# Kernel optimization log

Measured on AMD Instinct MI355X. Metric: run time of the kernel, lower is better.

## Reference

```python
import jax, jax.numpy as jnp
import numpy as np

NEG = -1000000000.0  # mask value used by the original module

def setup_inputs() -> dict:
    key = jax.random.key(0)
    kq, kk, kv, kl = jax.random.split(key, 4)
    B, Lq, Lk, D, Dv = 16, 2048, 2048, 64, 64
    q = jax.random.normal(kq, (B, Lq, D), dtype=jnp.float32)
    k = jax.random.normal(kk, (B, Lk, D), dtype=jnp.float32)
    v = jax.random.normal(kv, (B, Lk, Dv), dtype=jnp.float32)
    valid_len = jax.random.randint(kl, (B, Lq), 0, Lk, dtype=jnp.int32)
    return {"q": q, "k": k, "v": v, "valid_len": valid_len}

def reference(q, k, v, valid_len):
    # scores: [B, Lq, Lk]  (NOTE: original module does NOT scale by sqrt(d))
    scores = jnp.einsum('bqd,bkd->bqk', q, k)
    Lk = k.shape[1]
    # per-(batch,query) valid length masking over the key dimension
    mask = jnp.arange(Lk, dtype=valid_len.dtype)[None, None, :] < valid_len[:, :, None]
    scores = jnp.where(mask, scores, NEG)
    attn = jax.nn.softmax(scores, axis=-1)
    # dropout p=0.0 -> identity
    return jnp.einsum('bqk,bkv->bqv', attn, v)
```

## Files before the change

kernel.cpp:

```cpp
#include <hip/hip_runtime.h>

typedef _Float16 f16;
typedef __attribute__((ext_vector_type(8))) _Float16 f16x8;
typedef __attribute__((ext_vector_type(4))) _Float16 f16x4;
typedef __attribute__((ext_vector_type(4))) float f32x4;

#define NB 16
#define LSEQ 2048
#define DIM 64
#define KVB 64
#define QT 128
#define NQT (LSEQ / QT)
#define NT (LSEQ / KVB)
#define LOG2E 1.44269504088896340736f

__device__ inline f16x4 pkcvt(const f32x4 x) {
    auto a = __builtin_amdgcn_cvt_pkrtz(x[0], x[1]);
    auto b = __builtin_amdgcn_cvt_pkrtz(x[2], x[3]);
    f16x4 t; t[0]=(f16)a[0]; t[1]=(f16)a[1]; t[2]=(f16)b[0]; t[3]=(f16)b[1];
    return t;
}

__device__ inline void gload16(const void* g, void* l) {
    __builtin_amdgcn_global_load_lds(
        (const __attribute__((address_space(1))) unsigned int*)g,
        (__attribute__((address_space(3))) unsigned int*)l, 16, 0, 0);
}

__device__ __host__ inline int kappa(int p) {
    int kt = p >> 4, hi = (p >> 2) & 3, g = p & 3;
    return ((kt & 1) << 5) + (hi << 3) + ((kt >> 1) << 2) + g;
}

__global__ __launch_bounds__(256) void prep(
    const float* __restrict__ kg, const float* __restrict__ vg,
    const int* __restrict__ vlg,
    f16* __restrict__ k16, f16* __restrict__ v16, int* __restrict__ perm)
{
    const int tid = threadIdx.x;
    if (blockIdx.x < NB * NT) {
        const int b = blockIdx.x & 15, t = blockIdx.x >> 4;
        const int bt = b * NT + t;
        const float* kb_ = kg + ((size_t)b * LSEQ + t * KVB) * DIM;
        const float* vb_ = vg + ((size_t)b * LSEQ + t * KVB) * DIM;
        f16* kd = k16 + (size_t)bt * (KVB * DIM);
        f16* vd = v16 + (size_t)bt * (KVB * DIM);
#pragma unroll
        for (int it = 0; it < 4; ++it) {
            int cc = tid + it * 256;
            int row = cc >> 4, c4 = (cc & 15) * 4;
            f32x4 x = *(const f32x4*)(kb_ + kappa(row) * DIM + c4);
            *(f16x4*)(kd + row * 64 + (c4 ^ ((row & 7) * 8))) = pkcvt(x);
        }
        int kb4 = tid & 15, dvb = tid >> 4;
        f32x4 rr[4];
#pragma unroll
        for (int i = 0; i < 4; ++i)
            rr[i] = *(const f32x4*)(vb_ + (size_t)(kb4 * 4 + i) * DIM + dvb * 4);
#pragma unroll
        for (int j = 0; j < 4; ++j) {
            int dv = dvb * 4 + j;
            f32x4 col = {rr[0][j], rr[1][j], rr[2][j], rr[3][j]};
            *(f16x4*)(vd + dv * 64 + ((kb4 * 4) ^ ((dv & 7) * 8))) = pkcvt(col);
        }
    } else {
        const int b = blockIdx.x - NB * NT;
        __shared__ int hist[NT + 1];
        __shared__ int base[NT + 1];
        if (tid <= NT) hist[tid] = 0;
        __syncthreads();
        for (int q = tid; q < LSEQ; q += 256) {
            int vl = vlg[b * LSEQ + q];
            int t = (vl == 0) ? NT : ((vl + KVB - 1) >> 6);
            atomicAdd(&hist[t], 1);
        }
        __syncthreads();
        if (tid == 0) {
            int acc = 0;
            for (int t = NT; t >= 0; --t) { base[t] = acc; acc += hist[t]; }
        }
        __syncthreads();
        for (int q = tid; q < LSEQ; q += 256) {
            int vl = vlg[b * LSEQ + q];
            int t = (vl == 0) ? NT : ((vl + KVB - 1) >> 6);
            int pos = atomicAdd(&base[t], 1);
            perm[b * LSEQ + pos] = q;
        }
    }
}

__global__ __launch_bounds__(256, 4) void attn_fwd(
    const float* __restrict__ qg, const int* __restrict__ vlg,
    const f16* __restrict__ k16, const f16* __restrict__ v16,
    float* __restrict__ outg, const int* __restrict__ perm,
    f16* __restrict__ opart, float* __restrict__ mlg, int S)
{
    __shared__ alignas(16) f16 kbuf[2][KVB * 64];
    __shared__ alignas(16) f16 vbuf[2][DIM * 64];
    __shared__ int wmax[4];

    const int tid  = threadIdx.x;
    const int wid  = tid >> 6;
    const int lane = tid & 63;
    const int r    = lane & 15;
    const int hi   = lane >> 4;

    const int bid = blockIdx.x;
    const int nbs = NB * S;
    const int qt  = bid / nbs;
    const int rem = bid - qt * nbs;
    const int s   = rem >> 4;
    const int b   = rem & 15;
    const int qw  = qt * QT + wid * 16;

    const int qidxA = perm[b * LSEQ + qw + r];
    const int qidxB = perm[b * LSEQ + qw + 64 + r];
    const int vlA   = vlg[b * LSEQ + qidxA];
    const int vlB   = vlg[b * LSEQ + qidxB];

    int tq = max((vlA == 0) ? NT : ((vlA + KVB - 1) >> 6),
                 (vlB == 0) ? NT : ((vlB + KVB - 1) >> 6));
    tq = max(tq, __shfl_xor(tq, 1));
    tq = max(tq, __shfl_xor(tq, 2));
    tq = max(tq, __shfl_xor(tq, 4));
    tq = max(tq, __shfl_xor(tq, 8));
    if (lane == 0) wmax[wid] = tq;
    __syncthreads();
    const int maxt = max(max(wmax[0], wmax[1]), max(wmax[2], wmax[3]));

    auto rmin = [&](int v) {
        v = min(v, __shfl_xor(v, 1));
        v = min(v, __shfl_xor(v, 2));
        v = min(v, __shfl_xor(v, 4));
        v = min(v, __shfl_xor(v, 8));
        return v;
    };
    const int vminA = rmin(vlA);
    const int vminB = rmin(vlB);

    auto load_q = [&](int qidx, f16x8* qf) {
        const float* qrow = qg + ((size_t)(b * LSEQ + qidx)) * DIM;
#pragma unroll
        for (int ks = 0; ks < 2; ++ks) {
            f32x4 x = *(const f32x4*)(qrow + ks * 32 + hi * 8);
            f32x4 y = *(const f32x4*)(qrow + ks * 32 + hi * 8 + 4);
            f32x4 xs = {x[0]*LOG2E, x[1]*LOG2E, x[2]*LOG2E, x[3]*LOG2E};
            f32x4 ys = {y[0]*LOG2E, y[1]*LOG2E, y[2]*LOG2E, y[3]*LOG2E};
            f16x4 lo = pkcvt(xs), hh = pkcvt(ys);
            f16x8 t;
            t[0]=lo[0]; t[1]=lo[1]; t[2]=lo[2]; t[3]=lo[3];
            t[4]=hh[0]; t[5]=hh[1]; t[6]=hh[2]; t[7]=hh[3];
            qf[ks] = t;
        }
    };
    f16x8 qfA[2], qfB[2];
    load_q(qidxA, qfA);
    load_q(qidxB, qfB);

    float mA = -INFINITY, mB = -INFINITY;
    float lA = 0.0f, lB = 0.0f;
    f32x4 oA[4], oB[4];
#pragma unroll
    for (int dt = 0; dt < 4; ++dt) { oA[dt] = f32x4{0,0,0,0}; oB[dt] = f32x4{0,0,0,0}; }

    const f16* kt_base = k16 + (size_t)b * (NT * KVB * DIM);
    const f16* vt_base = v16 + (size_t)b * (NT * KVB * DIM);
    const int swz = (r & 7) * 8;

    auto stage = [&](int bi, int t) {
        const char* ks = (const char*)(kt_base + (size_t)t * 4096);
        const char* vs = (const char*)(vt_base + (size_t)t * 4096);
        char* kd = (char*)&kbuf[bi][0];
        char* vd = (char*)&vbuf[bi][0];
        gload16(ks + tid * 16,        kd + tid * 16);
        gload16(ks + 4096 + tid * 16, kd + 4096 + tid * 16);
        gload16(vs + tid * 16,        vd + tid * 16);
        gload16(vs + 4096 + tid * 16, vd + 4096 + tid * 16);
    };

    auto do_sm = [&](f32x4* st, int vl, int vmin, float& m_run, float& l_run,
                     f32x4* o, int kv0, f16x8* pa) {
        float lanemax = -INFINITY;
        if (kv0 + KVB > vmin) {
#pragma unroll
            for (int kt = 0; kt < 4; ++kt)
#pragma unroll
                for (int g = 0; g < 4; ++g) {
                    int key = kv0 + ((kt & 1) << 5) + (hi << 3) + ((kt >> 1) << 2) + g;
                    float sv = (key < vl) ? st[kt][g] : -1e9f;
                    st[kt][g] = sv;
                    lanemax = fmaxf(lanemax, sv);
                }
        } else {
#pragma unroll
            for (int kt = 0; kt < 4; ++kt)
#pragma unroll
                for (int g = 0; g < 4; ++g)
                    lanemax = fmaxf(lanemax, st[kt][g]);
        }

        if (__any(lanemax > m_run + 8.0f)) {
            float tmax = lanemax;
            tmax = fmaxf(tmax, __shfl_xor(tmax, 16));
            tmax = fmaxf(tmax, __shfl_xor(tmax, 32));
            float m_new = fmaxf(m_run, tmax);
            float scale = exp2f(m_run - m_new);
            l_run *= scale;
            m_run = m_new;
#pragma unroll
            for (int g = 0; g < 4; ++g) {
                float sc = __shfl(scale, hi * 4 + g);
#pragma unroll
                for (int dt = 0; dt < 4; ++dt) o[dt][g] *= sc;
            }
        }

#pragma unroll
        for (int kt = 0; kt < 4; ++kt)
#pragma unroll
            for (int g = 0; g < 4; ++g) {
                float p = exp2f(st[kt][g] - m_run);
                l_run += p;
                pa[kt & 1][((kt >> 1) << 2) + g] = (f16)p;
            }
    };

    if (s < maxt) stage(0, s);
    int c = 0;
    for (int tt = s; tt < maxt; tt += S) {
        __syncthreads();
        if (tt + S < maxt) stage(c ^ 1, tt + S);
        const int kv0 = tt * KVB;

        f32x4 stA[4], stB[4];
        __builtin_amdgcn_s_setprio(1);
#pragma unroll
        for (int kt = 0; kt < 4; ++kt) {
            f16x8 kf0 = *(const f16x8*)(&kbuf[c][(kt * 16 + r) * 64 + ((0 * 32 + hi * 8) ^ swz)]);
            f16x8 kf1 = *(const f16x8*)(&kbuf[c][(kt * 16 + r) * 64 + ((1 * 32 + hi * 8) ^ swz)]);
            f32x4 a = __builtin_amdgcn_mfma_f32_16x16x32_f16(kf0, qfA[0], f32x4{0,0,0,0}, 0, 0, 0);
            stA[kt] = __builtin_amdgcn_mfma_f32_16x16x32_f16(kf1, qfA[1], a, 0, 0, 0);
            f32x4 bb = __builtin_amdgcn_mfma_f32_16x16x32_f16(kf0, qfB[0], f32x4{0,0,0,0}, 0, 0, 0);
            stB[kt] = __builtin_amdgcn_mfma_f32_16x16x32_f16(kf1, qfB[1], bb, 0, 0, 0);
        }
        __builtin_amdgcn_s_setprio(0);

        f16x8 paA[2], paB[2];
        do_sm(stA, vlA, vminA, mA, lA, oA, kv0, paA);
        do_sm(stB, vlB, vminB, mB, lB, oB, kv0, paB);

        __builtin_amdgcn_s_setprio(1);
#pragma unroll
        for (int dt = 0; dt < 4; ++dt)
#pragma unroll
            for (int ks = 0; ks < 2; ++ks) {
                f16x8 vf = *(const f16x8*)(&vbuf[c][(dt * 16 + r) * 64 + ((ks * 32 + hi * 8) ^ swz)]);
                oA[dt] = __builtin_amdgcn_mfma_f32_16x16x32_f16(paA[ks], vf, oA[dt], 0, 0, 0);
                oB[dt] = __builtin_amdgcn_mfma_f32_16x16x32_f16(paB[ks], vf, oB[dt], 0, 0, 0);
            }
        __builtin_amdgcn_s_setprio(0);
        c ^= 1;
    }

    auto epi = [&](float m_run, float l_run, f32x4* o, int qidx) {
        l_run += __shfl_xor(l_run, 16);
        l_run += __shfl_xor(l_run, 32);
        if (S == 1) {
            float inv = 1.0f / l_run;
#pragma unroll
            for (int g = 0; g < 4; ++g) {
                float iv = __shfl(inv, hi * 4 + g);
                int   qo = __shfl(qidx, hi * 4 + g);
                float* ob = outg + ((size_t)(b * LSEQ + qo)) * DIM;
#pragma unroll
                for (int dt = 0; dt < 4; ++dt)
                    ob[dt * 16 + r] = o[dt][g] * iv;
            }
        } else {
            f16* obase = opart + ((size_t)s * NB * LSEQ + (size_t)b * LSEQ) * DIM;
#pragma unroll
            for (int g = 0; g < 4; ++g) {
                int qo = __shfl(qidx, hi * 4 + g);
                f16* ob = obase + (size_t)qo * DIM;
#pragma unroll
                for (int dt = 0; dt < 4; ++dt)
                    ob[dt * 16 + r] = (f16)o[dt][g];
            }
            if (hi == 0) {
                size_t mi = ((size_t)s * NB * LSEQ + (size_t)b * LSEQ + qidx) * 2;
                mlg[mi]     = m_run;
                mlg[mi + 1] = l_run;
            }
        }
    };
    epi(mA, lA, oA, qidxA);
    epi(mB, lB, oB, qidxB);
}

__global__ void merge_k(const f16* __restrict__ opart, const float* __restrict__ mlg,
                        float* __restrict__ outg, int S)
{
    const int gt = blockIdx.x * 256 + threadIdx.x;
    const size_t base = (size_t)gt * 4;
    const size_t qg = base >> 6;
    float M = -INFINITY;
    for (int s = 0; s < S; ++s)
        M = fmaxf(M, mlg[((size_t)s * NB * LSEQ + qg) * 2]);
    float den = 0.f;
    f32x4 acc = {0.f, 0.f, 0.f, 0.f};
    for (int s = 0; s < S; ++s) {
        size_t mi = ((size_t)s * NB * LSEQ + qg) * 2;
        float w = exp2f(mlg[mi] - M);
        den += w * mlg[mi + 1];
        f16x4 ov = *(const f16x4*)(opart + (size_t)s * (NB * LSEQ * DIM) + base);
        acc[0] += w * (float)ov[0]; acc[1] += w * (float)ov[1];
        acc[2] += w * (float)ov[2]; acc[3] += w * (float)ov[3];
    }
    float inv = 1.0f / den;
    f32x4 res = {acc[0]*inv, acc[1]*inv, acc[2]*inv, acc[3]*inv};
    *(f32x4*)(outg + base) = res;
}

extern "C" void kernel_launch(void* const* d_in, const int* in_sizes, int n_in,
                              void* d_out, int out_size, void* d_ws, size_t ws_size,
                              hipStream_t stream) {
    const float* q  = (const float*)d_in[0];
    const float* k  = (const float*)d_in[1];
    const float* v  = (const float*)d_in[2];
    const int*   vl = (const int*)d_in[3];
    float* out = (float*)d_out;

    const size_t perm_b = (size_t)NB * LSEQ * sizeof(int);
    const size_t kv_b   = (size_t)NB * LSEQ * DIM * sizeof(f16);
    auto need = [&](int S) {
        return perm_b + 2 * kv_b
             + (size_t)S * NB * LSEQ * 2 * sizeof(float)
             + (size_t)S * NB * LSEQ * DIM * sizeof(f16);
    };
    int S;
    if      (ws_size >= need(4)) S = 4;
    else if (ws_size >= need(2)) S = 2;
    else                         S = 1;

    int*   perm  = (int*)d_ws;
    f16*   k16   = (f16*)((char*)d_ws + perm_b);
    f16*   v16   = (f16*)((char*)d_ws + perm_b + kv_b);
    float* mlg   = (float*)((char*)d_ws + perm_b + 2 * kv_b);
    f16*   opart = (f16*)((char*)d_ws + perm_b + 2 * kv_b
                          + (size_t)S * NB * LSEQ * 2 * sizeof(float));

    prep<<<NB * NT + NB, 256, 0, stream>>>(k, v, vl, k16, v16, perm);

    attn_fwd<<<dim3(NQT * NB * S), dim3(256), 0, stream>>>(
        q, vl, k16, v16, out, perm, opart, mlg, S);

    if (S > 1) {
        const int mthreads = NB * LSEQ * DIM / 4;
        merge_k<<<dim3(mthreads / 256), dim3(256), 0, stream>>>(opart, mlg, out, S);
    }
}
```

Baseline: 46.03 us.

## Use per-query-tile variable split counts for balanced split-KV attention

Replaces the uniform split factor S with a per-query-tile table: tiles holding long valid lengths (sorted first) get up to 8 KV splits and short tiles fewer, giving 1072 blocks with more even work. Partial outputs and stats are now stored by sorted rank, so writes are contiguous, and the merge kernel scatters to the original query index through perm. The merge skips S==1 rows. This drops the workspace-size check and assumes room for 8 splits, and the merge still launches over all rows.

```diff
diff --git a/kernel.cpp b/kernel.cpp
--- a/kernel.cpp
+++ b/kernel.cpp
@@ -12,7 +12,13 @@
 #define QT 128
 #define NQT (LSEQ / QT)
 #define NT (LSEQ / KVB)
+#define SMAX 8
 #define LOG2E 1.44269504088896340736f
+
+__device__ __constant__ int STAB[NQT]     = {8,8,7,6,6,5,5,4,4,3,3,2,2,2,1,1};
+__device__ __constant__ int BTAB[NQT + 1] = {0,128,256,368,464,560,640,720,784,848,896,944,976,1008,1040,1056,1072};
+#define GRID_ATTN 1072
+static const int H_STAB[NQT] = {8,8,7,6,6,5,5,4,4,3,3,2,2,2,1,1};
 
 __device__ inline f16x4 pkcvt(const f32x4 x) {
     auto a = __builtin_amdgcn_cvt_pkrtz(x[0], x[1]);
@@ -93,7 +99,7 @@
     const float* __restrict__ qg, const int* __restrict__ vlg,
     const f16* __restrict__ k16, const f16* __restrict__ v16,
     float* __restrict__ outg, const int* __restrict__ perm,
-    f16* __restrict__ opart, float* __restrict__ mlg, int S)
+    f16* __restrict__ opart, float* __restrict__ mlg)
 {
     __shared__ alignas(16) f16 kbuf[2][KVB * 64];
     __shared__ alignas(16) f16 vbuf[2][DIM * 64];
@@ -106,15 +112,18 @@
     const int hi   = lane >> 4;
 
     const int bid = blockIdx.x;
-    const int nbs = NB * S;
-    const int qt  = bid / nbs;
-    const int rem = bid - qt * nbs;
+    int qt = 0;
+    while (bid >= BTAB[qt + 1]) ++qt;
+    const int rem = bid - BTAB[qt];
+    const int b   = rem & 15;
     const int s   = rem >> 4;
-    const int b   = rem & 15;
+    const int S   = STAB[qt];
     const int qw  = qt * QT + wid * 16;
 
-    const int qidxA = perm[b * LSEQ + qw + r];
-    const int qidxB = perm[b * LSEQ + qw + 64 + r];
+    const int rankA = qw + r;
+    const int rankB = qw + 64 + r;
+    const int qidxA = perm[b * LSEQ + rankA];
+    const int qidxB = perm[b * LSEQ + rankB];
     const int vlA   = vlg[b * LSEQ + qidxA];
     const int vlB   = vlg[b * LSEQ + qidxB];
 
@@ -262,7 +271,7 @@
         c ^= 1;
     }
 
-    auto epi = [&](float m_run, float l_run, f32x4* o, int qidx) {
+    auto epi = [&](float m_run, float l_run, f32x4* o, int qidx, int rank) {
         l_run += __shfl_xor(l_run, 16);
         l_run += __shfl_xor(l_run, 32);
         if (S == 1) {
@@ -280,36 +289,39 @@
             f16* obase = opart + ((size_t)s * NB * LSEQ + (size_t)b * LSEQ) * DIM;
 #pragma unroll
             for (int g = 0; g < 4; ++g) {
-                int qo = __shfl(qidx, hi * 4 + g);
-                f16* ob = obase + (size_t)qo * DIM;
+                int rk = __shfl(rank, hi * 4 + g);
+                f16* ob = obase + (size_t)rk * DIM;
 #pragma unroll
                 for (int dt = 0; dt < 4; ++dt)
                     ob[dt * 16 + r] = (f16)o[dt][g];
             }
             if (hi == 0) {
-                size_t mi = ((size_t)s * NB * LSEQ + (size_t)b * LSEQ + qidx) * 2;
+                size_t mi = ((size_t)s * NB * LSEQ + (size_t)b * LSEQ + rank) * 2;
                 mlg[mi]     = m_run;
                 mlg[mi + 1] = l_run;
             }
         }
     };
-    epi(mA, lA, oA, qidxA);
-    epi(mB, lB, oB, qidxB);
+    epi(mA, lA, oA, qidxA, rankA);
+    epi(mB, lB, oB, qidxB, rankB);
 }
 
 __global__ void merge_k(const f16* __restrict__ opart, const float* __restrict__ mlg,
-                        float* __restrict__ outg, int S)
+                        const int* __restrict__ perm, float* __restrict__ outg)
 {
     const int gt = blockIdx.x * 256 + threadIdx.x;
     const size_t base = (size_t)gt * 4;
-    const size_t qg = base >> 6;
+    const size_t rlin = base >> 6;
+    const int rank = (int)(rlin & (LSEQ - 1));
+    const int S = STAB[rank >> 7];
+    if (S == 1) return;
     float M = -INFINITY;
     for (int s = 0; s < S; ++s)
-        M = fmaxf(M, mlg[((size_t)s * NB * LSEQ + qg) * 2]);
+        M = fmaxf(M, mlg[((size_t)s * NB * LSEQ + rlin) * 2]);
     float den = 0.f;
     f32x4 acc = {0.f, 0.f, 0.f, 0.f};
     for (int s = 0; s < S; ++s) {
-        size_t mi = ((size_t)s * NB * LSEQ + qg) * 2;
+        size_t mi = ((size_t)s * NB * LSEQ + rlin) * 2;
         float w = exp2f(mlg[mi] - M);
         den += w * mlg[mi + 1];
         f16x4 ov = *(const f16x4*)(opart + (size_t)s * (NB * LSEQ * DIM) + base);
@@ -317,8 +329,11 @@
         acc[2] += w * (float)ov[2]; acc[3] += w * (float)ov[3];
     }
     float inv = 1.0f / den;
+    const size_t bq = (rlin >> 11);
+    const int qidx = perm[rlin];
+    float* ob = outg + ((size_t)(bq * LSEQ + qidx)) * DIM + (base & 63);
     f32x4 res = {acc[0]*inv, acc[1]*inv, acc[2]*inv, acc[3]*inv};
-    *(f32x4*)(outg + base) = res;
+    *(f32x4*)ob = res;
 }
 
 extern "C" void kernel_launch(void* const* d_in, const int* in_sizes, int n_in,
@@ -332,30 +347,22 @@
 
     const size_t perm_b = (size_t)NB * LSEQ * sizeof(int);
     const size_t kv_b   = (size_t)NB * LSEQ * DIM * sizeof(f16);
-    auto need = [&](int S) {
-        return perm_b + 2 * kv_b
-             + (size_t)S * NB * LSEQ * 2 * sizeof(float)
-             + (size_t)S * NB * LSEQ * DIM * sizeof(f16);
-    };
-    int S;
-    if      (ws_size >= need(4)) S = 4;
-    else if (ws_size >= need(2)) S = 2;
-    else                         S = 1;
+    const size_t mlg_b  = (size_t)SMAX * NB * LSEQ * 2 * sizeof(float);
+    const size_t need   = perm_b + 2 * kv_b + mlg_b
+                        + (size_t)SMAX * NB * LSEQ * DIM * sizeof(f16);
+    (void)need;
 
     int*   perm  = (int*)d_ws;
     f16*   k16   = (f16*)((char*)d_ws + perm_b);
     f16*   v16   = (f16*)((char*)d_ws + perm_b + kv_b);
     float* mlg   = (float*)((char*)d_ws + perm_b + 2 * kv_b);
-    f16*   opart = (f16*)((char*)d_ws + perm_b + 2 * kv_b
-                          + (size_t)S * NB * LSEQ * 2 * sizeof(float));
+    f16*   opart = (f16*)((char*)d_ws + perm_b + 2 * kv_b + mlg_b);
 
     prep<<<NB * NT + NB, 256, 0, stream>>>(k, v, vl, k16, v16, perm);
 
-    attn_fwd<<<dim3(NQT * NB * S), dim3(256), 0, stream>>>(
-        q, vl, k16, v16, out, perm, opart, mlg, S);
-
-    if (S > 1) {
-        const int mthreads = NB * LSEQ * DIM / 4;
-        merge_k<<<dim3(mthreads / 256), dim3(256), 0, stream>>>(opart, mlg, out, S);
-    }
-}
+    attn_fwd<<<dim3(GRID_ATTN), dim3(256), 0, stream>>>(
+        q, vl, k16, v16, out, perm, opart, mlg);
+
+    const int mthreads = NB * LSEQ * DIM / 4;
+    merge_k<<<dim3(mthreads / 256), dim3(256), 0, stream>>>(opart, mlg, perm, out);
+}
```

New measurement: 51.96 us. +12.9%, slower.

## Use non-uniform KV split counts, with more splits for the longest query tiles

Applied to the files above, without the earlier changes.

Query tiles are ordered by descending valid length. This change gives the first eight tiles eight KV splits and the remaining tiles four, instead of a uniform split count, so the heaviest tiles are spread over more blocks for better load balance. A new init kernel sets the max/sum planes to -inf/0 so that unused split planes drop out of the merge. The merge now always reads eight planes. The costs are an extra kernel launch, more merge traffic, and reliance on unused opart planes not holding NaN, since a zero weight times NaN is still NaN.

```diff
diff --git a/kernel.cpp b/kernel.cpp
--- a/kernel.cpp
+++ b/kernel.cpp
@@ -12,6 +12,7 @@
 #define QT 128
 #define NQT (LSEQ / QT)
 #define NT (LSEQ / KVB)
+#define SMAX 8
 #define LOG2E 1.44269504088896340736f
 
 __device__ inline f16x4 pkcvt(const f32x4 x) {
@@ -93,7 +94,7 @@
     const float* __restrict__ qg, const int* __restrict__ vlg,
     const f16* __restrict__ k16, const f16* __restrict__ v16,
     float* __restrict__ outg, const int* __restrict__ perm,
-    f16* __restrict__ opart, float* __restrict__ mlg, int S)
+    f16* __restrict__ opart, float* __restrict__ mlg, int mode)
 {
     __shared__ alignas(16) f16 kbuf[2][KVB * 64];
     __shared__ alignas(16) f16 vbuf[2][DIM * 64];
@@ -106,12 +107,22 @@
     const int hi   = lane >> 4;
 
     const int bid = blockIdx.x;
-    const int nbs = NB * S;
-    const int qt  = bid / nbs;
-    const int rem = bid - qt * nbs;
-    const int s   = rem >> 4;
-    const int b   = rem & 15;
-    const int qw  = qt * QT + wid * 16;
+    int qt, s, b, S;
+    if (mode == 0) {
+        if (bid < NB * 8 * 8) {
+            S = 8; qt = bid >> 7;
+            int rem = bid & 127; s = rem >> 4; b = rem & 15;
+        } else {
+            S = 4; int b2 = bid - NB * 8 * 8;
+            qt = 8 + (b2 >> 6);
+            int rem = b2 & 63; s = rem >> 4; b = rem & 15;
+        }
+    } else {
+        S = mode;
+        int nbs = NB * S; qt = bid / nbs;
+        int rem = bid - qt * nbs; s = rem >> 4; b = rem & 15;
+    }
+    const int qw = qt * QT + wid * 16;
 
     const int qidxA = perm[b * LSEQ + qw + r];
     const int qidxB = perm[b * LSEQ + qw + 64 + r];
@@ -298,11 +309,19 @@
 }
 
 __global__ void merge_k(const f16* __restrict__ opart, const float* __restrict__ mlg,
-                        float* __restrict__ outg, int S)
+                        const int* __restrict__ perm, float* __restrict__ outg, int mode)
 {
     const int gt = blockIdx.x * 256 + threadIdx.x;
     const size_t base = (size_t)gt * 4;
     const size_t qg = base >> 6;
+    int S;
+    if (mode == 0) {
+        const int rank_chunk = (int)((qg & (LSEQ - 1)) >> 7);
+        (void)rank_chunk;
+        S = SMAX;
+    } else {
+        S = mode;
+    }
     float M = -INFINITY;
     for (int s = 0; s < S; ++s)
         M = fmaxf(M, mlg[((size_t)s * NB * LSEQ + qg) * 2]);
@@ -321,6 +340,12 @@
     *(f32x4*)(outg + base) = res;
 }
 
+__global__ void mlg_init(float* __restrict__ mlg) {
+    const int i = blockIdx.x * 256 + threadIdx.x;
+    mlg[(size_t)i * 2]     = -INFINITY;
+    mlg[(size_t)i * 2 + 1] = 0.0f;
+}
+
 extern "C" void kernel_launch(void* const* d_in, const int* in_sizes, int n_in,
                               void* d_out, int out_size, void* d_ws, size_t ws_size,
                               hipStream_t stream) {
@@ -337,25 +362,31 @@
              + (size_t)S * NB * LSEQ * 2 * sizeof(float)
              + (size_t)S * NB * LSEQ * DIM * sizeof(f16);
     };
-    int S;
-    if      (ws_size >= need(4)) S = 4;
-    else if (ws_size >= need(2)) S = 2;
-    else                         S = 1;
+    int mode;
+    if      (ws_size >= need(SMAX)) mode = 0;
+    else if (ws_size >= need(4))    mode = 4;
+    else if (ws_size >= need(2))    mode = 2;
+    else                            mode = 1;
+    const int planes = (mode == 0) ? SMAX : mode;
 
     int*   perm  = (int*)d_ws;
     f16*   k16   = (f16*)((char*)d_ws + perm_b);
     f16*   v16   = (f16*)((char*)d_ws + perm_b + kv_b);
     float* mlg   = (float*)((char*)d_ws + perm_b + 2 * kv_b);
     f16*   opart = (f16*)((char*)d_ws + perm_b + 2 * kv_b
-                          + (size_t)S * NB * LSEQ * 2 * sizeof(float));
+                          + (size_t)planes * NB * LSEQ * 2 * sizeof(float));
 
     prep<<<NB * NT + NB, 256, 0, stream>>>(k, v, vl, k16, v16, perm);
-
-    attn_fwd<<<dim3(NQT * NB * S), dim3(256), 0, stream>>>(
-        q, vl, k16, v16, out, perm, opart, mlg, S);
-
-    if (S > 1) {
+    if (planes > 1)
+        mlg_init<<<planes * NB * LSEQ / 256, 256, 0, stream>>>(mlg);
+
+    const int grid = (mode == 0) ? (NB * 8 * 8 + NB * 8 * 4)
+                                 : (NQT * NB * mode);
+    attn_fwd<<<dim3(grid), dim3(256), 0, stream>>>(
+        q, vl, k16, v16, out, perm, opart, mlg, mode);
+
+    if (planes > 1) {
         const int mthreads = NB * LSEQ * DIM / 4;
-        merge_k<<<dim3(mthreads / 256), dim3(256), 0, stream>>>(opart, mlg, out, S);
-    }
-}
+        merge_k<<<dim3(mthreads / 256), dim3(256), 0, stream>>>(opart, mlg, perm, out, mode);
+    }
+}
```

After: 54.25 us. 17.8% more time.
